# Kernel tuning notes

Hardware: AMD Instinct MI355X
Metric: run time of the kernel (lower is better)

The kernel has to match this reference:

```python
import jax, jax.numpy as jnp
import numpy as np

B, N, BR, BC = 1024, 9, 3, 3
L = N * N                 # 81 cells
D, H, F = 512, 8, 2048
E = D // H                # 64 head dim
EPS = 1e-5


def _layernorm(x, g, b):
    m = jnp.mean(x, axis=-1, keepdims=True)
    v = jnp.mean(jnp.square(x - m), axis=-1, keepdims=True)
    return (x - m) * jax.lax.rsqrt(v + EPS) * g + b


def setup_inputs() -> dict:
    key = jax.random.key(0)
    ks = jax.random.split(key, 14)
    s = 0.02
    return {
        "src":   jax.random.normal(ks[0], (B, L, D), jnp.float32),
        # linear weights stored as (in, out) so y = x @ W + b (same math as torch x @ W.T + b)
        "w_qkv": jax.random.normal(ks[1], (D, 3 * D), jnp.float32) * s,
        "b_qkv": jnp.zeros((3 * D,), jnp.float32),
        "w_out": jax.random.normal(ks[2], (D, D), jnp.float32) * s,
        "b_out": jnp.zeros((D,), jnp.float32),
        "g1": jnp.ones((D,), jnp.float32),
        "beta1": jnp.zeros((D,), jnp.float32),
        "g2": jnp.ones((D,), jnp.float32),
        "beta2": jnp.zeros((D,), jnp.float32),
        "w_ff1": jax.random.normal(ks[3], (D, F), jnp.float32) * s,
        "b_ff1": jnp.zeros((F,), jnp.float32),
        "w_ff2": jax.random.normal(ks[4], (F, D), jnp.float32) * s,
        "b_ff2": jnp.zeros((D,), jnp.float32),
    }


def reference(src, w_qkv, b_qkv, w_out, b_out, g1, beta1, g2, beta2,
              w_ff1, b_ff1, w_ff2, b_ff2):
    # pre-norm attention
    x = _layernorm(src, g1, beta1)
    qkv = x @ w_qkv + b_qkv                       # (B, L, 3D)
    q, k, v = jnp.split(qkv, 3, axis=-1)
    rs = lambda t: t.reshape(B, N, N, H, E)       # (B, row, col, H, E)
    q2, k2, v2 = rs(q), rs(k), rs(v)
    scale = 1.0 / np.sqrt(E).astype(np.float32)

    # row attention: attend over columns within each row
    s_r = jnp.einsum('brqhe,brkhe->brhqk', q2, k2) * scale
    y_r = jnp.einsum('brhqk,brkhe->brqhe', jax.nn.softmax(s_r, axis=-1), v2)

    # column attention: attend over rows within each column
    s_c = jnp.einsum('bqche,bkche->bchqk', q2, k2) * scale
    y_c = jnp.einsum('bchqk,bkche->bqche', jax.nn.softmax(s_c, axis=-1), v2)

    # block attention: attend within each 3x3 block (9 cells)
    n_br, n_bc = N // BR, N // BC
    blk = lambda t: (t.reshape(B, n_br, BR, n_bc, BC, H, E)
                      .transpose(0, 1, 3, 2, 4, 5, 6)
                      .reshape(B, n_br, n_bc, BR * BC, H, E))
    qb, kb, vb = blk(q2), blk(k2), blk(v2)
    s_b = jnp.einsum('bijqhe,bijkhe->bijhqk', qb, kb) * scale
    y_b = jnp.einsum('bijhqk,bijkhe->bijqhe', jax.nn.softmax(s_b, axis=-1), vb)
    y_b = (y_b.reshape(B, n_br, n_bc, BR, BC, H, E)
              .transpose(0, 1, 3, 2, 4, 5, 6)
              .reshape(B, N, N, H, E))

    y = (y_r + y_c + y_b) / 3.0
    y = y.reshape(B, L, D) @ w_out + b_out

    x = src + y                                   # dropout = 0 (eval)
    residual = x
    h = _layernorm(x, g2, beta2)
    h = jax.nn.gelu(h @ w_ff1 + b_ff1, approximate=False) @ w_ff2 + b_ff2
    return residual + h
```

## Files before the change

### kernel.cpp

```cpp
#include <hip/hip_runtime.h>

#define BB 1024
#define NN 9
#define LL 81
#define DD 512
#define HH 8
#define EE 64
#define FF 2048
#define MM (BB*LL)
#define N3 (3*DD)

typedef unsigned short u16;
typedef __bf16 bf16x8 __attribute__((ext_vector_type(8)));
typedef float f32x4 __attribute__((ext_vector_type(4)));
typedef unsigned short u16x8 __attribute__((ext_vector_type(8)));

__device__ __forceinline__ float bf2f(u16 u) {
    return __uint_as_float(((unsigned int)u) << 16);
}
__device__ __forceinline__ u16 f2bf(float f) {
    unsigned int u = __float_as_uint(f);
    unsigned int r = u + 0x7fffu + ((u >> 16) & 1u);
    return (u16)(r >> 16);
}
__device__ __forceinline__ float gelu_exact(float v) {
    return 0.5f * v * (1.0f + erff(v * 0.70710678118654752f));
}

#define GL16(g, l) __builtin_amdgcn_global_load_lds( \
    (const __attribute__((address_space(1))) void*)(g), \
    (__attribute__((address_space(3))) void*)(l), 16, 0, 0)

#define SB0 __builtin_amdgcn_sched_barrier(0)

__global__ void transpose_w(const float* __restrict__ W, u16* __restrict__ Wt,
                            int K, int N) {
    __shared__ float t[32][33];
    int n0 = blockIdx.x * 32, k0 = blockIdx.y * 32;
    int tx = threadIdx.x & 31, ty = threadIdx.x >> 5;
#pragma unroll
    for (int i = 0; i < 32; i += 8)
        t[ty + i][tx] = W[(long)(k0 + ty + i) * N + n0 + tx];
    __syncthreads();
#pragma unroll
    for (int i = 0; i < 32; i += 8)
        Wt[(long)(n0 + ty + i) * K + k0 + tx] = f2bf(t[tx][ty + i]);
}

__global__ __launch_bounds__(256) void layernorm_k(const float* __restrict__ X,
                                                   const float* __restrict__ g,
                                                   const float* __restrict__ be,
                                                   u16* __restrict__ Y) {
    int row = blockIdx.x * 4 + (threadIdx.x >> 6);
    int lane = threadIdx.x & 63;
    const float4* xp = (const float4*)(X + (long)row * DD);
    float4 a = xp[lane * 2], b = xp[lane * 2 + 1];
    float s  = a.x + a.y + a.z + a.w + b.x + b.y + b.z + b.w;
    float sq = a.x*a.x + a.y*a.y + a.z*a.z + a.w*a.w
             + b.x*b.x + b.y*b.y + b.z*b.z + b.w*b.w;
#pragma unroll
    for (int off = 1; off < 64; off <<= 1) {
        s  += __shfl_xor(s, off);
        sq += __shfl_xor(sq, off);
    }
    float mean = s * (1.0f / 512.0f);
    float var  = sq * (1.0f / 512.0f) - mean * mean;
    float rstd = rsqrtf(var + 1e-5f);
    const float4* gp = (const float4*)(g + lane * 8);
    const float4* bp = (const float4*)(be + lane * 8);
    float4 g0 = gp[0], g1v = gp[1], b0 = bp[0], b1v = bp[1];
    float xv[8] = {a.x,a.y,a.z,a.w,b.x,b.y,b.z,b.w};
    float gv[8] = {g0.x,g0.y,g0.z,g0.w,g1v.x,g1v.y,g1v.z,g1v.w};
    float bv[8] = {b0.x,b0.y,b0.z,b0.w,b1v.x,b1v.y,b1v.z,b1v.w};
    u16x8 ov;
#pragma unroll
    for (int j = 0; j < 8; ++j)
        ov[j] = f2bf((xv[j] - mean) * rstd * gv[j] + bv[j]);
    *(u16x8*)(Y + (long)row * DD + lane * 8) = ov;
}

enum { EPI_BF16_BIAS = 0, EPI_F32_RESID = 1, EPI_BF16_GELU = 2, EPI_F32_ACCUM = 3 };

template <int EPI>
__global__ __launch_bounds__(256, 3) void gemm_bt(
    const u16* __restrict__ A, int lda,
    const u16* __restrict__ Bt, int ldb,
    const float* __restrict__ bias,
    const float* __restrict__ resid,
    u16* __restrict__ outB, float* __restrict__ outF,
    int N, int K, int nbn) {
    __shared__ u16 smem[24576];
    u16* const Asb = smem;
    u16* const Bsb = smem + 12288;
    const int tid = threadIdx.x;
    const int lane = tid & 63;
    const int w = tid >> 6;
    const int wr = w >> 1, wc = w & 1;

    const int cpx = gridDim.x >> 3;
    const int bid = (blockIdx.x & 7) * cpx + (blockIdx.x >> 3);
    const int bm = bid / nbn, bn = bid % nbn;
    const long Arow0 = (long)bm * 128;
    const long Brow0 = (long)bn * 128;

    auto stage = [&](int buf, int kt) {
        const u16* abase = A + Arow0 * (long)lda + (long)kt * 32;
        const u16* bbase = Bt + Brow0 * (long)ldb + (long)kt * 32;
#pragma unroll
        for (int u = 0; u < 2; ++u) {
            const int c = tid + u * 256;
            const int row = c >> 2;
            const int col = ((c & 3) ^ ((row >> 1) & 3)) * 8;
            GL16(abase + (long)row * lda + col, Asb + buf * 4096 + c * 8);
            GL16(bbase + (long)row * ldb + col, Bsb + buf * 4096 + c * 8);
        }
    };

    f32x4 acc[4][4] = {};
    const int fr = lane & 15;
    const int s8 = lane >> 4;
    const int sl = (s8 ^ ((fr >> 1) & 3)) * 8;

    const int nk = K / 32;
    stage(0, 0); stage(1, 1);

    int cur = 0;
    for (int kt = 0; kt < nk; ++kt) {
        if (kt + 1 < nk) { asm volatile("s_waitcnt vmcnt(4)" ::: "memory"); }
        else             { asm volatile("s_waitcnt vmcnt(0)" ::: "memory"); }
        SB0;
        __builtin_amdgcn_s_barrier();
        SB0;

        bf16x8 af[4], bb[4];
        const u16* Ab = Asb + cur * 4096;
        const u16* Bb = Bsb + cur * 4096;
#pragma unroll
        for (int mt = 0; mt < 4; ++mt)
            af[mt] = *(const bf16x8*)(Ab + (wr * 64 + mt * 16 + fr) * 32 + sl);
#pragma unroll
        for (int nt = 0; nt < 4; ++nt)
            bb[nt] = *(const bf16x8*)(Bb + (wc * 64 + nt * 16 + fr) * 32 + sl);

        if (kt + 2 < nk) {
            int nb = cur + 2; if (nb >= 3) nb -= 3;
            stage(nb, kt + 2);
        }

        asm volatile("s_waitcnt lgkmcnt(0)" ::: "memory");
        SB0;
#pragma unroll
        for (int mt = 0; mt < 4; ++mt)
#pragma unroll
            for (int nt = 0; nt < 4; ++nt)
                acc[mt][nt] = __builtin_amdgcn_mfma_f32_16x16x32_bf16(af[mt], bb[nt], acc[mt][nt], 0, 0, 0);
        cur = cur + 1; if (cur == 3) cur = 0;
    }

    if (EPI == EPI_BF16_BIAS || EPI == EPI_BF16_GELU) {
        __builtin_amdgcn_s_barrier();
        u16 (*eps)[132] = (u16(*)[132])smem;
#pragma unroll
        for (int nt = 0; nt < 4; ++nt) {
            const int cl = wc * 64 + nt * 16 + fr;
            const float bv = bias ? bias[bn * 128 + cl] : 0.0f;
#pragma unroll
            for (int mt = 0; mt < 4; ++mt) {
                const int rl = wr * 64 + mt * 16 + s8 * 4;
#pragma unroll
                for (int q = 0; q < 4; ++q) {
                    float v = acc[mt][nt][q] + bv;
                    if (EPI == EPI_BF16_GELU) v = gelu_exact(v);
                    eps[rl + q][cl] = f2bf(v);
                }
            }
        }
        __syncthreads();
#pragma unroll
        for (int u = 0; u < 8; ++u) {
            const int i = u * 256 + tid;
            const int row = i >> 4, cc = (i & 15) * 8;
            u16x8 vv = *(const u16x8*)&eps[row][cc];
            *(u16x8*)(outB + (Arow0 + row) * (long)N + bn * 128 + cc) = vv;
        }
    } else {
        const int col0 = bn * 128 + wc * 64;
        const int row0 = bm * 128 + wr * 64;
#pragma unroll
        for (int nt = 0; nt < 4; ++nt) {
            const int col = col0 + nt * 16 + fr;
            const float bv = bias ? bias[col] : 0.0f;
#pragma unroll
            for (int mt = 0; mt < 4; ++mt) {
                const int rowb = row0 + mt * 16 + s8 * 4;
#pragma unroll
                for (int q = 0; q < 4; ++q) {
                    const long idx = (long)(rowb + q) * N + col;
                    float v = acc[mt][nt][q] + bv;
                    if (EPI == EPI_F32_RESID) outF[idx] = v + resid[idx];
                    else                      outF[idx] += v;
                }
            }
        }
    }
}

__global__ __launch_bounds__(256) void attn_k(const u16* __restrict__ qkv,
                                              u16* __restrict__ y) {
    __shared__ u16 S[96][104];
    __shared__ u16 Wm[96][104];
    __shared__ u16 Vt[64][104];
    const int bh = blockIdx.x;
    const int b = bh >> 3, h = bh & 7;
    const u16* qbase = qkv + (long)b * LL * N3 + h * EE;
    const u16* kbase = qbase + DD;
    const u16* vbase = qbase + 2 * DD;
    const int tid = threadIdx.x;
    const int lane = tid & 63;
    const int w = tid >> 6;
    const int fr = lane & 15, s8 = lane >> 4;

    {
        u16x8 z = {};
        u16* wp = &Wm[0][0];
        for (int i = tid; i < (96 * 104) / 8; i += 256)
            *(u16x8*)(wp + i * 8) = z;
        for (int i = tid; i < 64 * 16; i += 256) {
            int e = i >> 4, c = i & 15;
            if (c < 15) Vt[e][81 + c] = 0;
        }
        for (int i = tid; i < 81 * 16; i += 256) {
            int cell = i >> 4, e0 = (i & 15) * 4;
            ushort4 v = *(const ushort4*)(vbase + (long)cell * N3 + e0);
            Vt[e0][cell] = v.x; Vt[e0 + 1][cell] = v.y;
            Vt[e0 + 2][cell] = v.z; Vt[e0 + 3][cell] = v.w;
        }
    }

    for (int i = 0; i < 9; ++i) {
        const int tile = w + 4 * i;
        const int qt = tile / 6, kt = tile % 6;
        int qc = qt * 16 + fr; if (qc > 80) qc = 80;
        int kc = kt * 16 + fr; if (kc > 80) kc = 80;
        const u16* qp = qbase + (long)qc * N3 + s8 * 8;
        const u16* kp = kbase + (long)kc * N3 + s8 * 8;
        bf16x8 a0 = *(const bf16x8*)qp;
        bf16x8 a1 = *(const bf16x8*)(qp + 32);
        bf16x8 b0 = *(const bf16x8*)kp;
        bf16x8 b1 = *(const bf16x8*)(kp + 32);
        f32x4 acc = {};
        acc = __builtin_amdgcn_mfma_f32_16x16x32_bf16(a0, b0, acc, 0, 0, 0);
        acc = __builtin_amdgcn_mfma_f32_16x16x32_bf16(a1, b1, acc, 0, 0, 0);
#pragma unroll
        for (int q = 0; q < 4; ++q)
            S[qt * 16 + s8 * 4 + q][kt * 16 + fr] = f2bf(acc[q]);
    }
    __syncthreads();

    if (tid < 81) {
        const int q = tid;
        const int r = q / 9, c = q % 9;
#pragma unroll
        for (int t = 0; t < 3; ++t) {
            int mm[9];
            if (t == 0) {
#pragma unroll
                for (int j = 0; j < 9; ++j) mm[j] = r * 9 + j;
            } else if (t == 1) {
#pragma unroll
                for (int j = 0; j < 9; ++j) mm[j] = j * 9 + c;
            } else {
                const int br = (r / 3) * 3, bc = (c / 3) * 3;
#pragma unroll
                for (int j = 0; j < 9; ++j) mm[j] = (br + j / 3) * 9 + bc + j % 3;
            }
            float sc[9], mx = -1e30f;
#pragma unroll
            for (int j = 0; j < 9; ++j) {
                sc[j] = bf2f(S[q][mm[j]]) * 0.125f;
                mx = fmaxf(mx, sc[j]);
            }
            float sum = 0.0f;
#pragma unroll
            for (int j = 0; j < 9; ++j) { sc[j] = __expf(sc[j] - mx); sum += sc[j]; }
            const float inv = 1.0f / (3.0f * sum);
#pragma unroll
            for (int j = 0; j < 9; ++j) {
                u16* p = &Wm[q][mm[j]];
                *p = f2bf(bf2f(*p) + sc[j] * inv);
            }
        }
    }
    __syncthreads();

    for (int i = 0; i < 6; ++i) {
        const int tile = w + 4 * i;
        const int qt = tile % 6, et = tile / 6;
        f32x4 acc = {};
#pragma unroll
        for (int kc = 0; kc < 3; ++kc) {
            bf16x8 a  = *(const bf16x8*)&Vt[et * 16 + fr][kc * 32 + s8 * 8];
            bf16x8 bf = *(const bf16x8*)&Wm[qt * 16 + fr][kc * 32 + s8 * 8];
            acc = __builtin_amdgcn_mfma_f32_16x16x32_bf16(a, bf, acc, 0, 0, 0);
        }
        const int q = qt * 16 + fr;
        if (q < 81) {
            ushort4 o;
            o.x = f2bf(acc[0]); o.y = f2bf(acc[1]);
            o.z = f2bf(acc[2]); o.w = f2bf(acc[3]);
            *(ushort4*)(y + (long)(b * LL + q) * DD + h * EE + et * 16 + s8 * 4) = o;
        }
    }
}

extern "C" void kernel_launch(void* const* d_in, const int* in_sizes, int n_in,
                              void* d_out, int out_size, void* d_ws, size_t ws_size,
                              hipStream_t stream) {
    const float* src    = (const float*)d_in[0];
    const float* w_qkv  = (const float*)d_in[1];
    const float* b_qkv  = (const float*)d_in[2];
    const float* w_out  = (const float*)d_in[3];
    const float* b_out  = (const float*)d_in[4];
    const float* g1     = (const float*)d_in[5];
    const float* beta1  = (const float*)d_in[6];
    const float* g2     = (const float*)d_in[7];
    const float* beta2  = (const float*)d_in[8];
    const float* w_ff1  = (const float*)d_in[9];
    const float* b_ff1  = (const float*)d_in[10];
    const float* w_ff2  = (const float*)d_in[11];
    const float* b_ff2  = (const float*)d_in[12];
    float* out = (float*)d_out;

    char* ws = (char*)d_ws;
    u16* wqkvt = (u16*)(ws + 0);
    u16* woutt = (u16*)(ws + 1572864);
    u16* wff1t = (u16*)(ws + 2097152);
    u16* wff2t = (u16*)(ws + 4194304);
    u16* bufA  = (u16*)(ws + 6291456);
    u16* bufB  = (u16*)(ws + 6291456 + 84934656ULL);
    u16* hln   = bufB;
    u16* h1    = bufB + (size_t)MM * DD;

    const int nbm = MM / 128;
    const int nbmh = (MM / 2) / 128;

    transpose_w<<<dim3(N3 / 32, DD / 32), 256, 0, stream>>>(w_qkv, wqkvt, DD, N3);
    transpose_w<<<dim3(DD / 32, DD / 32), 256, 0, stream>>>(w_out, woutt, DD, DD);
    transpose_w<<<dim3(FF / 32, DD / 32), 256, 0, stream>>>(w_ff1, wff1t, DD, FF);
    transpose_w<<<dim3(DD / 32, FF / 32), 256, 0, stream>>>(w_ff2, wff2t, FF, DD);

    layernorm_k<<<MM / 4, 256, 0, stream>>>(src, g1, beta1, bufA);

    gemm_bt<EPI_BF16_BIAS><<<nbm * (N3 / 128), 256, 0, stream>>>(
        bufA, DD, wqkvt, DD, b_qkv, nullptr, bufB, nullptr, N3, DD, N3 / 128);

    attn_k<<<BB * HH, 256, 0, stream>>>(bufB, bufA);

    gemm_bt<EPI_F32_RESID><<<nbm * (DD / 128), 256, 0, stream>>>(
        bufA, DD, woutt, DD, b_out, src, nullptr, out, DD, DD, DD / 128);

    layernorm_k<<<MM / 4, 256, 0, stream>>>(out, g2, beta2, hln);

    for (int mh = 0; mh < 2; ++mh) {
        const size_t roff = (size_t)mh * (MM / 2);
        gemm_bt<EPI_BF16_GELU><<<nbmh * (FF / 128), 256, 0, stream>>>(
            hln + roff * DD, DD, wff1t, DD, b_ff1, nullptr,
            h1, nullptr, FF, DD, FF / 128);
        gemm_bt<EPI_F32_ACCUM><<<nbmh * (DD / 128), 256, 0, stream>>>(
            h1, FF, wff2t, FF, b_ff2, nullptr,
            nullptr, out + roff * DD, DD, FF, DD / 128);
    }
}
```

Baseline: 1.206 ms.

## Use 256x128 GEMM tiles, keep the residual in bf16, write attention output in place

```diff
diff --git a/kernel.cpp b/kernel.cpp
--- a/kernel.cpp
+++ b/kernel.cpp
@@ -79,19 +79,53 @@
     *(u16x8*)(Y + (long)row * DD + lane * 8) = ov;
 }
 
-enum { EPI_BF16_BIAS = 0, EPI_F32_RESID = 1, EPI_BF16_GELU = 2, EPI_F32_ACCUM = 3 };
+__global__ __launch_bounds__(256) void layernorm_b(const u16* __restrict__ X,
+                                                   const float* __restrict__ g,
+                                                   const float* __restrict__ be,
+                                                   u16* __restrict__ Y) {
+    int row = blockIdx.x * 4 + (threadIdx.x >> 6);
+    int lane = threadIdx.x & 63;
+    u16x8 xr = *(const u16x8*)(X + (long)row * DD + lane * 8);
+    float xv[8];
+#pragma unroll
+    for (int j = 0; j < 8; ++j) xv[j] = bf2f(xr[j]);
+    float s = 0.0f, sq = 0.0f;
+#pragma unroll
+    for (int j = 0; j < 8; ++j) { s += xv[j]; sq += xv[j] * xv[j]; }
+#pragma unroll
+    for (int off = 1; off < 64; off <<= 1) {
+        s  += __shfl_xor(s, off);
+        sq += __shfl_xor(sq, off);
+    }
+    float mean = s * (1.0f / 512.0f);
+    float var  = sq * (1.0f / 512.0f) - mean * mean;
+    float rstd = rsqrtf(var + 1e-5f);
+    const float4* gp = (const float4*)(g + lane * 8);
+    const float4* bp = (const float4*)(be + lane * 8);
+    float4 g0 = gp[0], g1v = gp[1], b0 = bp[0], b1v = bp[1];
+    float gv[8] = {g0.x,g0.y,g0.z,g0.w,g1v.x,g1v.y,g1v.z,g1v.w};
+    float bv[8] = {b0.x,b0.y,b0.z,b0.w,b1v.x,b1v.y,b1v.z,b1v.w};
+    u16x8 ov;
+#pragma unroll
+    for (int j = 0; j < 8; ++j)
+        ov[j] = f2bf((xv[j] - mean) * rstd * gv[j] + bv[j]);
+    *(u16x8*)(Y + (long)row * DD + lane * 8) = ov;
+}
+
+enum { EPI_BF16_BIAS = 0, EPI_BF16_RESID = 1, EPI_BF16_GELU = 2, EPI_F32_XADD = 3 };
 
 template <int EPI>
-__global__ __launch_bounds__(256, 3) void gemm_bt(
+__global__ __launch_bounds__(256, 2) void gemm_bt(
     const u16* __restrict__ A, int lda,
     const u16* __restrict__ Bt, int ldb,
     const float* __restrict__ bias,
-    const float* __restrict__ resid,
+    const float* __restrict__ residF,
+    const u16* __restrict__ residB,
     u16* __restrict__ outB, float* __restrict__ outF,
     int N, int K, int nbn) {
-    __shared__ u16 smem[24576];
+    __shared__ u16 smem[36864];
     u16* const Asb = smem;
-    u16* const Bsb = smem + 12288;
+    u16* const Bsb = smem + 24576;
     const int tid = threadIdx.x;
     const int lane = tid & 63;
     const int w = tid >> 6;
@@ -100,23 +134,29 @@
     const int cpx = gridDim.x >> 3;
     const int bid = (blockIdx.x & 7) * cpx + (blockIdx.x >> 3);
     const int bm = bid / nbn, bn = bid % nbn;
-    const long Arow0 = (long)bm * 128;
+    const long Arow0 = (long)bm * 256;
     const long Brow0 = (long)bn * 128;
 
     auto stage = [&](int buf, int kt) {
         const u16* abase = A + Arow0 * (long)lda + (long)kt * 32;
         const u16* bbase = Bt + Brow0 * (long)ldb + (long)kt * 32;
+#pragma unroll
+        for (int u = 0; u < 4; ++u) {
+            const int c = tid + u * 256;
+            const int row = c >> 2;
+            const int col = ((c & 3) ^ ((row >> 1) & 3)) * 8;
+            GL16(abase + (long)row * lda + col, Asb + buf * 8192 + c * 8);
+        }
 #pragma unroll
         for (int u = 0; u < 2; ++u) {
             const int c = tid + u * 256;
             const int row = c >> 2;
             const int col = ((c & 3) ^ ((row >> 1) & 3)) * 8;
-            GL16(abase + (long)row * lda + col, Asb + buf * 4096 + c * 8);
             GL16(bbase + (long)row * ldb + col, Bsb + buf * 4096 + c * 8);
         }
     };
 
-    f32x4 acc[4][4] = {};
+    f32x4 acc[8][4] = {};
     const int fr = lane & 15;
     const int s8 = lane >> 4;
     const int sl = (s8 ^ ((fr >> 1) & 3)) * 8;
@@ -126,18 +166,18 @@
 
     int cur = 0;
     for (int kt = 0; kt < nk; ++kt) {
-        if (kt + 1 < nk) { asm volatile("s_waitcnt vmcnt(4)" ::: "memory"); }
+        if (kt + 1 < nk) { asm volatile("s_waitcnt vmcnt(6)" ::: "memory"); }
         else             { asm volatile("s_waitcnt vmcnt(0)" ::: "memory"); }
         SB0;
         __builtin_amdgcn_s_barrier();
         SB0;
 
-        bf16x8 af[4], bb[4];
-        const u16* Ab = Asb + cur * 4096;
+        bf16x8 af[8], bb[4];
+        const u16* Ab = Asb + cur * 8192;
         const u16* Bb = Bsb + cur * 4096;
 #pragma unroll
-        for (int mt = 0; mt < 4; ++mt)
-            af[mt] = *(const bf16x8*)(Ab + (wr * 64 + mt * 16 + fr) * 32 + sl);
+        for (int mt = 0; mt < 8; ++mt)
+            af[mt] = *(const bf16x8*)(Ab + (wr * 128 + mt * 16 + fr) * 32 + sl);
 #pragma unroll
         for (int nt = 0; nt < 4; ++nt)
             bb[nt] = *(const bf16x8*)(Bb + (wc * 64 + nt * 16 + fr) * 32 + sl);
@@ -150,14 +190,14 @@
         asm volatile("s_waitcnt lgkmcnt(0)" ::: "memory");
         SB0;
 #pragma unroll
-        for (int mt = 0; mt < 4; ++mt)
+        for (int mt = 0; mt < 8; ++mt)
 #pragma unroll
             for (int nt = 0; nt < 4; ++nt)
                 acc[mt][nt] = __builtin_amdgcn_mfma_f32_16x16x32_bf16(af[mt], bb[nt], acc[mt][nt], 0, 0, 0);
         cur = cur + 1; if (cur == 3) cur = 0;
     }
 
-    if (EPI == EPI_BF16_BIAS || EPI == EPI_BF16_GELU) {
+    if (EPI == EPI_BF16_BIAS || EPI == EPI_BF16_GELU || EPI == EPI_BF16_RESID) {
         __builtin_amdgcn_s_barrier();
         u16 (*eps)[132] = (u16(*)[132])smem;
 #pragma unroll
@@ -165,19 +205,21 @@
             const int cl = wc * 64 + nt * 16 + fr;
             const float bv = bias ? bias[bn * 128 + cl] : 0.0f;
 #pragma unroll
-            for (int mt = 0; mt < 4; ++mt) {
-                const int rl = wr * 64 + mt * 16 + s8 * 4;
+            for (int mt = 0; mt < 8; ++mt) {
+                const int rl = wr * 128 + mt * 16 + s8 * 4;
 #pragma unroll
                 for (int q = 0; q < 4; ++q) {
                     float v = acc[mt][nt][q] + bv;
                     if (EPI == EPI_BF16_GELU) v = gelu_exact(v);
+                    if (EPI == EPI_BF16_RESID)
+                        v += residF[(Arow0 + rl + q) * (long)N + bn * 128 + cl];
                     eps[rl + q][cl] = f2bf(v);
                 }
             }
         }
         __syncthreads();
 #pragma unroll
-        for (int u = 0; u < 8; ++u) {
+        for (int u = 0; u < 16; ++u) {
             const int i = u * 256 + tid;
             const int row = i >> 4, cc = (i & 15) * 8;
             u16x8 vv = *(const u16x8*)&eps[row][cc];
@@ -185,34 +227,31 @@
         }
     } else {
         const int col0 = bn * 128 + wc * 64;
-        const int row0 = bm * 128 + wr * 64;
+        const long row0 = Arow0 + wr * 128;
 #pragma unroll
         for (int nt = 0; nt < 4; ++nt) {
             const int col = col0 + nt * 16 + fr;
             const float bv = bias ? bias[col] : 0.0f;
 #pragma unroll
-            for (int mt = 0; mt < 4; ++mt) {
-                const int rowb = row0 + mt * 16 + s8 * 4;
+            for (int mt = 0; mt < 8; ++mt) {
+                const long rowb = row0 + mt * 16 + s8 * 4;
 #pragma unroll
                 for (int q = 0; q < 4; ++q) {
-                    const long idx = (long)(rowb + q) * N + col;
-                    float v = acc[mt][nt][q] + bv;
-                    if (EPI == EPI_F32_RESID) outF[idx] = v + resid[idx];
-                    else                      outF[idx] += v;
+                    const long idx = (rowb + q) * N + col;
+                    outF[idx] = acc[mt][nt][q] + bv + bf2f(residB[idx]);
                 }
             }
         }
     }
 }
 
-__global__ __launch_bounds__(256) void attn_k(const u16* __restrict__ qkv,
-                                              u16* __restrict__ y) {
+__global__ __launch_bounds__(256) void attn_k(u16* __restrict__ qkv) {
     __shared__ u16 S[96][104];
     __shared__ u16 Wm[96][104];
     __shared__ u16 Vt[64][104];
     const int bh = blockIdx.x;
     const int b = bh >> 3, h = bh & 7;
-    const u16* qbase = qkv + (long)b * LL * N3 + h * EE;
+    u16* qbase = qkv + (long)b * LL * N3 + h * EE;
     const u16* kbase = qbase + DD;
     const u16* vbase = qbase + 2 * DD;
     const int tid = threadIdx.x;
@@ -308,7 +347,7 @@
             ushort4 o;
             o.x = f2bf(acc[0]); o.y = f2bf(acc[1]);
             o.z = f2bf(acc[2]); o.w = f2bf(acc[3]);
-            *(ushort4*)(y + (long)(b * LL + q) * DD + h * EE + et * 16 + s8 * 4) = o;
+            *(ushort4*)(qbase + (long)q * N3 + et * 16 + s8 * 4) = o;
         }
     }
 }
@@ -341,8 +380,8 @@
     u16* hln   = bufB;
     u16* h1    = bufB + (size_t)MM * DD;
 
-    const int nbm = MM / 128;
-    const int nbmh = (MM / 2) / 128;
+    const int nbm  = MM / 256;
+    const int nbmh = (MM / 2) / 256;
 
     transpose_w<<<dim3(N3 / 32, DD / 32), 256, 0, stream>>>(w_qkv, wqkvt, DD, N3);
     transpose_w<<<dim3(DD / 32, DD / 32), 256, 0, stream>>>(w_out, woutt, DD, DD);
@@ -352,22 +391,22 @@
     layernorm_k<<<MM / 4, 256, 0, stream>>>(src, g1, beta1, bufA);
 
     gemm_bt<EPI_BF16_BIAS><<<nbm * (N3 / 128), 256, 0, stream>>>(
-        bufA, DD, wqkvt, DD, b_qkv, nullptr, bufB, nullptr, N3, DD, N3 / 128);
-
-    attn_k<<<BB * HH, 256, 0, stream>>>(bufB, bufA);
-
-    gemm_bt<EPI_F32_RESID><<<nbm * (DD / 128), 256, 0, stream>>>(
-        bufA, DD, woutt, DD, b_out, src, nullptr, out, DD, DD, DD / 128);
-
-    layernorm_k<<<MM / 4, 256, 0, stream>>>(out, g2, beta2, hln);
+        bufA, DD, wqkvt, DD, b_qkv, nullptr, nullptr, bufB, nullptr, N3, DD, N3 / 128);
+
+    attn_k<<<BB * HH, 256, 0, stream>>>(bufB);
+
+    gemm_bt<EPI_BF16_RESID><<<nbm * (DD / 128), 256, 0, stream>>>(
+        bufB, N3, woutt, DD, b_out, src, nullptr, bufA, nullptr, DD, DD, DD / 128);
+
+    layernorm_b<<<MM / 4, 256, 0, stream>>>(bufA, g2, beta2, hln);
 
     for (int mh = 0; mh < 2; ++mh) {
         const size_t roff = (size_t)mh * (MM / 2);
         gemm_bt<EPI_BF16_GELU><<<nbmh * (FF / 128), 256, 0, stream>>>(
-            hln + roff * DD, DD, wff1t, DD, b_ff1, nullptr,
+            hln + roff * DD, DD, wff1t, DD, b_ff1, nullptr, nullptr,
             h1, nullptr, FF, DD, FF / 128);
-        gemm_bt<EPI_F32_ACCUM><<<nbmh * (DD / 128), 256, 0, stream>>>(
-            h1, FF, wff2t, FF, b_ff2, nullptr,
+        gemm_bt<EPI_F32_XADD><<<nbmh * (DD / 128), 256, 0, stream>>>(
+            h1, FF, wff2t, FF, b_ff2, nullptr, bufA + roff * DD,
             nullptr, out + roff * DD, DD, FF, DD / 128);
     }
 }
```

Result: faster. 1.150 ms (-4.6%).
